# Kernel tuning notes

Hardware: AMD Instinct MI355X
Metric: run time of the kernel (lower is better)

The kernel has to match this reference:

```python
import jax, jax.numpy as jnp
import numpy as np

B, S, D, H, L = 8, 512, 1024, 16, 2
DH = D // H
EPS = 1e-6
SCALE = float(np.sqrt(DH))


def _ln(x, g, b):
    # custom LayerNormalization: unbiased std (torch default), eps added to std
    m = x.mean(axis=-1, keepdims=True)
    s = jnp.std(x, axis=-1, keepdims=True, ddof=1)
    return g * (x - m) / (s + EPS) + b


def _pos_encoding(seq_len, dim):
    pos = jnp.arange(seq_len, dtype=jnp.float32)[:, None]
    dims = jnp.arange(dim, dtype=jnp.float32)
    div = 10000.0 ** (2.0 * dims / dim)
    pe = jnp.zeros((seq_len, dim), jnp.float32)
    pe = pe.at[:, 0::2].set(jnp.sin(pos / div[0::2]))
    pe = pe.at[:, 1::2].set(jnp.cos(pos / div[1::2]))
    return pe


def setup_inputs() -> dict:
    key = jax.random.key(0)
    ks = jax.random.split(key, 20)
    std = 0.02
    p = lambda k, shape: jax.random.normal(k, shape, jnp.float32) * std
    return {
        "features": jax.random.normal(ks[0], (B, S, D), jnp.float32),
        "mask": jnp.ones((B, S), jnp.int32),
        "ln_in_g": jnp.ones((D,), jnp.float32),
        "ln_in_b": jnp.zeros((D,), jnp.float32),
        "Wq": p(ks[1], (L, D, D)), "bq": p(ks[2], (L, D)),
        "Wk": p(ks[3], (L, D, D)), "bk": p(ks[4], (L, D)),
        "Wv": p(ks[5], (L, D, D)), "bv": p(ks[6], (L, D)),
        "Wo": p(ks[7], (L, D, D)), "bo": p(ks[8], (L, D)),
        "ln1_g": jnp.ones((L, D), jnp.float32), "ln1_b": jnp.zeros((L, D), jnp.float32),
        "W1": p(ks[9], (L, D, D)), "b1": p(ks[10], (L, D)),
        "W2": p(ks[11], (L, D, D)), "b2": p(ks[12], (L, D)),
        "ln2_g": jnp.ones((L, D), jnp.float32), "ln2_b": jnp.zeros((L, D), jnp.float32),
    }


def reference(features, mask, ln_in_g, ln_in_b, Wq, bq, Wk, bk, Wv, bv, Wo, bo,
              ln1_g, ln1_b, W1, b1, W2, b2, ln2_g, ln2_b):
    # input norm + positional encoding (dropout inert at eval)
    x = _ln(features, ln_in_g, ln_in_b) + _pos_encoding(S, D)  # [B,S,D]
    # mask: positions where mask==0 are masked out with -1e18
    neg = (mask == 0)[:, None, None, :]  # [B,1,1,Sk]

    def encoder_layer(inp, i):
        q = (inp @ Wq[i].T + bq[i]).reshape(B, S, H, DH).transpose(0, 2, 1, 3)
        k = (inp @ Wk[i].T + bk[i]).reshape(B, S, H, DH).transpose(0, 2, 1, 3)
        v = (inp @ Wv[i].T + bv[i]).reshape(B, S, H, DH).transpose(0, 2, 1, 3)
        scores = jnp.einsum('bhqd,bhkd->bhqk', q, k) / SCALE
        scores = jnp.where(neg, -1e18, scores)
        attn = jax.nn.softmax(scores, axis=-1)
        ctx = jnp.einsum('bhqk,bhkd->bhqd', attn, v).transpose(0, 2, 1, 3).reshape(B, S, D)
        attn_out = ctx @ Wo[i].T + bo[i]
        s = _ln(attn_out + inp, ln1_g[i], ln1_b[i])  # residual + custom LN
        h = jax.nn.gelu(s @ W1[i].T + b1[i], approximate=False)
        f = h @ W2[i].T + b2[i]
        return _ln(f + s, ln2_g[i], ln2_b[i])

    # FAITHFUL to source: layers are NOT chained -- each layer reads the
    # original (query,key,value); output is the last layer's result.
    out = x
    for i in range(L):
        out = encoder_layer(x, i)
    return out
```

## Files before the change

### kernel.cpp

```cpp
#include <hip/hip_runtime.h>
#include <cstdint>
#include <cstddef>


typedef __attribute__((ext_vector_type(8))) short bf16x8;
typedef __attribute__((ext_vector_type(4))) short bf16x4;
typedef __attribute__((ext_vector_type(4))) float f32x4;

#define MFMA16(a, b, c) __builtin_amdgcn_mfma_f32_16x16x32_bf16((a), (b), (c), 0, 0, 0)

__device__ __forceinline__ unsigned short f2b(float f) {
  union { float f; unsigned int u; } x; x.f = f;
  unsigned int r = x.u + 0x7fffu + ((x.u >> 16) & 1u);
  return (unsigned short)(r >> 16);
}

__device__ __forceinline__ float b2f(unsigned short u) {
  union { unsigned int i; float f; } x;
  x.i = ((unsigned int)u) << 16;
  return x.f;
}

__device__ __forceinline__ void gl_lds16(const void* g, void* l) {
  __builtin_amdgcn_global_load_lds(
      (const __attribute__((address_space(1))) void*)g,
      (__attribute__((address_space(3))) void*)l, 16, 0, 0);
}

template <int BN, int EPI>
__global__ __launch_bounds__(256) void gemm_t(
    const unsigned short* __restrict__ A, const unsigned short* __restrict__ B,
    const float* __restrict__ bias, unsigned short* __restrict__ outB, int N,
    int K, int nnHalf) {
  extern __shared__ char smem[];
  char* la = smem;
  char* lb = smem + 3 * 16384;
  constexpr int NR = BN / 32;
  const int tid = threadIdx.x;
  const int l = tid & 63, w = tid >> 6;
  const int l15 = l & 15, l4 = l >> 4;
  const int xcd = blockIdx.x & 7, r = blockIdx.x >> 3;
  const int m0 = ((xcd >> 1) * 8 + (r & 7)) * 128;
  const int n0 = ((xcd & 1) * nnHalf + (r >> 3)) * BN;
  const int wr = (w >> 1) * 64, wc = (w & 1) * (BN / 2);
  const int NT = K >> 6;

#define STAGE(buf, t)                                                         \
  {                                                                           \
    const int k0_ = (t) * 64;                                                 \
    _Pragma("unroll") for (int i = 0; i < 4; ++i) {                           \
      const int c = i * 256 + tid;                                            \
      const int row = c >> 3;                                                 \
      const int gch = (c & 7) ^ (row & 7);                                    \
      gl_lds16(A + (size_t)(m0 + row) * K + k0_ + gch * 8,                    \
               la + (buf) * 16384 + (i * 256 + w * 64) * 16);                 \
    }                                                                         \
    _Pragma("unroll") for (int i = 0; i < BN / 32; ++i) {                     \
      const int c = i * 256 + tid;                                            \
      const int row = c >> 3;                                                 \
      const int gch = (c & 7) ^ (row & 7);                                    \
      gl_lds16(B + (size_t)(n0 + row) * K + k0_ + gch * 8,                    \
               lb + (buf) * (BN * 128) + (i * 256 + w * 64) * 16);            \
    }                                                                         \
  }
#define WAIT_L()                                                   \
  {                                                                \
    if constexpr (BN == 128) {                                     \
      asm volatile("s_waitcnt vmcnt(8)" ::: "memory");             \
    } else {                                                       \
      asm volatile("s_waitcnt vmcnt(6)" ::: "memory");             \
    }                                                              \
  }

  f32x4 acc[4][NR] = {};
  const int sw = l15 & 7;

  STAGE(0, 0);
  STAGE(1, 1);
  WAIT_L();
  __builtin_amdgcn_sched_barrier(0);
  __builtin_amdgcn_s_barrier();
  __builtin_amdgcn_sched_barrier(0);

  for (int t = 0; t < NT; ++t) {
    if (t + 2 < NT) {
      STAGE((t + 2) % 3, t + 2);
    }
    __builtin_amdgcn_sched_barrier(0);
    const char* abuf = la + (t % 3) * 16384;
    const char* bbuf = lb + (t % 3) * (BN * 128);
#pragma unroll
    for (int kk = 0; kk < 2; ++kk) {
      const unsigned int ch = (unsigned int)(((kk * 4 + l4) ^ sw) << 4);
      bf16x8 af[4], bfr[NR];
#pragma unroll
      for (int m = 0; m < 4; ++m)
        af[m] = *(const bf16x8*)(abuf + (wr + m * 16 + l15) * 128 + ch);
#pragma unroll
      for (int n = 0; n < NR; ++n)
        bfr[n] = *(const bf16x8*)(bbuf + (wc + n * 16 + l15) * 128 + ch);
#pragma unroll
      for (int m = 0; m < 4; ++m) {
#pragma unroll
        for (int n = 0; n < NR; ++n) {
          acc[m][n] = MFMA16(af[m], bfr[n], acc[m][n]);
        }
      }
    }
    if (t < NT - 1) {
      if (t + 2 < NT) {
        WAIT_L();
      } else {
        asm volatile("s_waitcnt vmcnt(0)" ::: "memory");
      }
      __builtin_amdgcn_sched_barrier(0);
      __builtin_amdgcn_s_barrier();
      __builtin_amdgcn_sched_barrier(0);
    }
  }
#undef STAGE
#undef WAIT_L

#pragma unroll
  for (int m = 0; m < 4; ++m) {
#pragma unroll
    for (int n = 0; n < NR; ++n) {
      const int col = n0 + wc + n * 16 + l15;
      const float bb = bias[col];
#pragma unroll
      for (int e = 0; e < 4; ++e) {
        const int row = m0 + wr + m * 16 + l4 * 4 + e;
        float v = acc[m][n][e] + bb;
        if (EPI == 1) {
          if (col < 1024) v *= 0.125f;
        } else if (EPI == 2) {
          v = 0.5f * v * (1.f + erff(v * 0.70710678118654752f));
        }
        outB[(size_t)row * N + col] = f2b(v);
      }
    }
  }
}

__global__ __launch_bounds__(256, 2) void attn_kernel(
    const unsigned short* __restrict__ qkv, const int* __restrict__ mask,
    unsigned short* __restrict__ ctx) {
  extern __shared__ char smem[];
  float* maskadd = (float*)(smem + 65536);
  const int bid = blockIdx.x;
  const int b = bid & 7, h = (bid >> 3) & 15, qt = bid >> 7;
  const int tid = threadIdx.x, l = tid & 63, w = tid >> 6;
  const int l15 = l & 15, l4 = l >> 4;
  const size_t RB = (size_t)b * 512 * 3072;

  for (int s = tid; s < 512; s += 256)
    maskadd[s] = mask[b * 512 + s] ? 0.f : -1e18f;

  const unsigned short* Kbase = qkv + RB + 1024 + h * 64;
  const unsigned short* Vbase = qkv + RB + 2048 + h * 64;

  const int kr0 = tid >> 2, kc0 = tid & 3;
  const unsigned int swzk = (unsigned int)((kr0 & 7) << 4);
  const unsigned int ka0 = ((unsigned int)(kr0 * 128 + kc0 * 16)) ^ swzk;
  const unsigned int ka1 = ((unsigned int)(kr0 * 128 + kc0 * 16 + 64)) ^ swzk;
  const int vs0 = 2 * l, vd0 = w * 16;

  bf16x8 k00, k01, k10, k11, vreg[4];
  k00 = *(const bf16x8*)(Kbase + (size_t)kr0 * 3072 + kc0 * 8);
  k01 = *(const bf16x8*)(Kbase + (size_t)kr0 * 3072 + kc0 * 8 + 32);
  k10 = *(const bf16x8*)(Kbase + (size_t)(kr0 + 64) * 3072 + kc0 * 8);
  k11 = *(const bf16x8*)(Kbase + (size_t)(kr0 + 64) * 3072 + kc0 * 8 + 32);
  vreg[0] = *(const bf16x8*)(Vbase + (size_t)vs0 * 3072 + vd0);
  vreg[1] = *(const bf16x8*)(Vbase + (size_t)vs0 * 3072 + vd0 + 8);
  vreg[2] = *(const bf16x8*)(Vbase + (size_t)(vs0 + 1) * 3072 + vd0);
  vreg[3] = *(const bf16x8*)(Vbase + (size_t)(vs0 + 1) * 3072 + vd0 + 8);

  const int q0 = qt * 64 + w * 16;
  const unsigned short* qb =
      qkv + RB + (size_t)(q0 + l15) * 3072 + h * 64 + l4 * 8;
  const bf16x8 qf0 = *(const bf16x8*)(qb);
  const bf16x8 qf1 = *(const bf16x8*)(qb + 32);

#define KWRITE(dst)                        \
  {                                        \
    *(bf16x8*)((dst) + ka0) = k00;         \
    *(bf16x8*)((dst) + ka1) = k01;         \
    *(bf16x8*)((dst) + ka0 + 8192) = k10;  \
    *(bf16x8*)((dst) + ka1 + 8192) = k11;  \
  }
#define VWRITE(dst)                                                          \
  {                                                                          \
    _Pragma("unroll") for (int j = 0; j < 16; ++j) {                         \
      const unsigned short lo_ =                                             \
          (unsigned short)((j < 8) ? vreg[0][j] : vreg[1][j - 8]);           \
      const unsigned short hi_ =                                             \
          (unsigned short)((j < 8) ? vreg[2][j] : vreg[3][j - 8]);           \
      *(unsigned int*)((dst) +                                               \
                       (((vd0 + j) * 256 + vs0 * 2) ^ ((j & 7) << 4))) =     \
          (unsigned int)lo_ | ((unsigned int)hi_ << 16);                     \
    }                                                                        \
  }

  KWRITE(smem);
  VWRITE(smem + 32768);
  __syncthreads();

  const int hi4 = l4 >> 1, gl = l4 & 1, g2 = l4 & 2;
  f32x4 acc[4] = {};
  float run_m = -1e30f, run_s = 0.f;

#pragma unroll
  for (int t = 0; t < 4; ++t) {
    char* kcur = smem + (t & 1) * 16384;
    char* vcur = smem + 32768 + (t & 1) * 16384;
    if (t < 3) {
      const int sn = (t + 1) * 128;
      k00 = *(const bf16x8*)(Kbase + (size_t)(sn + kr0) * 3072 + kc0 * 8);
      k01 = *(const bf16x8*)(Kbase + (size_t)(sn + kr0) * 3072 + kc0 * 8 + 32);
      k10 = *(const bf16x8*)(Kbase + (size_t)(sn + kr0 + 64) * 3072 + kc0 * 8);
      k11 = *(const bf16x8*)(Kbase + (size_t)(sn + kr0 + 64) * 3072 + kc0 * 8 + 32);
      vreg[0] = *(const bf16x8*)(Vbase + (size_t)(sn + vs0) * 3072 + vd0);
      vreg[1] = *(const bf16x8*)(Vbase + (size_t)(sn + vs0) * 3072 + vd0 + 8);
      vreg[2] = *(const bf16x8*)(Vbase + (size_t)(sn + vs0 + 1) * 3072 + vd0);
      vreg[3] = *(const bf16x8*)(Vbase + (size_t)(sn + vs0 + 1) * 3072 + vd0 + 8);
      __builtin_amdgcn_sched_barrier(0);
    }
    f32x4 sc[8];
    __builtin_amdgcn_s_setprio(1);
#pragma unroll
    for (int kk = 0; kk < 8; ++kk) {
      const unsigned int lin = (unsigned int)((kk * 16 + l15) * 128 + l4 * 16);
      const unsigned int swz = (unsigned int)((l15 & 7) << 4);
      const bf16x8 af0 = *(const bf16x8*)(kcur + (lin ^ swz));
      const bf16x8 af1 = *(const bf16x8*)(kcur + ((lin + 64) ^ swz));
      f32x4 c = {0.f, 0.f, 0.f, 0.f};
      c = MFMA16(af0, qf0, c);
      c = MFMA16(af1, qf1, c);
      sc[kk] = c;
    }
    __builtin_amdgcn_s_setprio(0);
    float tmx = -1e30f;
#pragma unroll
    for (int kk = 0; kk < 8; ++kk) {
#pragma unroll
      for (int e = 0; e < 4; ++e) {
        const float v = sc[kk][e] + maskadd[t * 128 + kk * 16 + l4 * 4 + e];
        sc[kk][e] = v;
        tmx = fmaxf(tmx, v);
      }
    }
    tmx = fmaxf(tmx, __shfl_xor(tmx, 16));
    tmx = fmaxf(tmx, __shfl_xor(tmx, 32));
    const float nm = (t == 0) ? tmx : fmaxf(run_m, tmx);
    float tsum = 0.f;
    unsigned int pk[8][2];
#pragma unroll
    for (int kk = 0; kk < 8; ++kk) {
      const float p0 = __expf(sc[kk][0] - nm);
      const float p1 = __expf(sc[kk][1] - nm);
      const float p2 = __expf(sc[kk][2] - nm);
      const float p3 = __expf(sc[kk][3] - nm);
      tsum += (p0 + p1) + (p2 + p3);
      asm("v_cvt_pk_bf16_f32 %0, %1, %2" : "=v"(pk[kk][0]) : "v"(p0), "v"(p1));
      asm("v_cvt_pk_bf16_f32 %0, %1, %2" : "=v"(pk[kk][1]) : "v"(p2), "v"(p3));
    }
    tsum += __shfl_xor(tsum, 16);
    tsum += __shfl_xor(tsum, 32);
    if (t == 0) {
      run_s = tsum;
    } else {
      const float scale = __expf(run_m - nm);
      run_s = run_s * scale + tsum;
      float s4[4];
#pragma unroll
      for (int e = 0; e < 4; ++e) s4[e] = __shfl(scale, l4 * 4 + e);
#pragma unroll
      for (int nt = 0; nt < 4; ++nt) {
#pragma unroll
        for (int e = 0; e < 4; ++e) acc[nt][e] *= s4[e];
      }
    }
    run_m = nm;
#pragma unroll
    for (int k2 = 0; k2 < 4; ++k2) {
      const unsigned int own0 = hi4 ? pk[2 * k2 + 1][0] : pk[2 * k2][0];
      const unsigned int own1 = hi4 ? pk[2 * k2 + 1][1] : pk[2 * k2][1];
      const unsigned int oth0 = hi4 ? pk[2 * k2][0] : pk[2 * k2 + 1][0];
      const unsigned int oth1 = hi4 ? pk[2 * k2][1] : pk[2 * k2 + 1][1];
      const unsigned int s16_0 = (unsigned int)__shfl_xor((int)own0, 16);
      const unsigned int s16_1 = (unsigned int)__shfl_xor((int)own1, 16);
      const unsigned int s32_0 = (unsigned int)__shfl_xor((int)oth0, 32);
      const unsigned int s32_1 = (unsigned int)__shfl_xor((int)oth1, 32);
      const unsigned int s48_0 = (unsigned int)__shfl_xor((int)oth0, 48);
      const unsigned int s48_1 = (unsigned int)__shfl_xor((int)oth1, 48);
      union { unsigned int u[4]; bf16x8 v; } pa;
      pa.u[0] = g2 ? (gl ? s16_0 : s32_0) : (gl ? s48_0 : own0);
      pa.u[1] = g2 ? (gl ? s16_1 : s32_1) : (gl ? s48_1 : own1);
      pa.u[2] = g2 ? (gl ? own0 : s48_0) : (gl ? s32_0 : s16_0);
      pa.u[3] = g2 ? (gl ? own1 : s48_1) : (gl ? s32_1 : s16_1);
      __builtin_amdgcn_s_setprio(1);
#pragma unroll
      for (int nt = 0; nt < 4; ++nt) {
        const int d = nt * 16 + l15;
        const unsigned int vb =
            (unsigned int)((d * 256 + k2 * 64 + l4 * 16) ^ ((l15 & 7) << 4));
        const bf16x8 vbf = *(const bf16x8*)(vcur + vb);
        acc[nt] = MFMA16(pa.v, vbf, acc[nt]);
      }
      __builtin_amdgcn_s_setprio(0);
    }
    if (t < 3) {
      char* knxt = smem + ((t + 1) & 1) * 16384;
      char* vnxt = smem + 32768 + ((t + 1) & 1) * 16384;
      KWRITE(knxt);
      VWRITE(vnxt);
      __syncthreads();
    }
  }
#undef KWRITE
#undef VWRITE

  const float inv = 1.f / run_s;
  float invq[4];
#pragma unroll
  for (int e = 0; e < 4; ++e) invq[e] = __shfl(inv, l4 * 4 + e);
#pragma unroll
  for (int nt = 0; nt < 4; ++nt) {
#pragma unroll
    for (int e = 0; e < 4; ++e) {
      const size_t row = (size_t)b * 512 + q0 + l4 * 4 + e;
      ctx[row * 1024 + h * 64 + nt * 16 + l15] = f2b(acc[nt][e] * invq[e]);
    }
  }
}

template <int MODE>
__global__ __launch_bounds__(256) void ln_k(
    const void* __restrict__ Ap, const void* __restrict__ Rp,
    const float* __restrict__ g, const float* __restrict__ bta,
    void* __restrict__ outp) {
  __shared__ float red[8];
  const int row = blockIdx.x, tid = threadIdx.x;
  const size_t base = (size_t)row * 1024 + tid * 4;
  float a4[4];
  {
    const bf16x4 a = *(const bf16x4*)((const unsigned short*)Ap + base);
    const bf16x4 rr = *(const bf16x4*)((const unsigned short*)Rp + base);
#pragma unroll
    for (int j = 0; j < 4; ++j)
      a4[j] = b2f((unsigned short)a[j]) + b2f((unsigned short)rr[j]);
  }
  float s = a4[0] + a4[1] + a4[2] + a4[3];
  float q = a4[0] * a4[0] + a4[1] * a4[1] + a4[2] * a4[2] + a4[3] * a4[3];
#pragma unroll
  for (int o = 32; o; o >>= 1) {
    s += __shfl_xor(s, o);
    q += __shfl_xor(q, o);
  }
  if ((tid & 63) == 0) {
    red[(tid >> 6) * 2] = s;
    red[(tid >> 6) * 2 + 1] = q;
  }
  __syncthreads();
  const float S = red[0] + red[2] + red[4] + red[6];
  const float Qs = red[1] + red[3] + red[5] + red[7];
  const float mean = S * (1.f / 1024.f);
  float var = (Qs - 1024.f * mean * mean) * (1.f / 1023.f);
  var = fmaxf(var, 0.f);
  const float inv = 1.f / (sqrtf(var) + 1e-6f);
  if (MODE == 2) {
    float4 o4;
    o4.x = g[tid * 4 + 0] * (a4[0] - mean) * inv + bta[tid * 4 + 0];
    o4.y = g[tid * 4 + 1] * (a4[1] - mean) * inv + bta[tid * 4 + 1];
    o4.z = g[tid * 4 + 2] * (a4[2] - mean) * inv + bta[tid * 4 + 2];
    o4.w = g[tid * 4 + 3] * (a4[3] - mean) * inv + bta[tid * 4 + 3];
    *(float4*)((float*)outp + base) = o4;
  } else {
    bf16x4 pb;
#pragma unroll
    for (int j = 0; j < 4; ++j) {
      const int col = tid * 4 + j;
      pb[j] = (short)f2b(g[col] * (a4[j] - mean) * inv + bta[col]);
    }
    *(bf16x4*)((unsigned short*)outp + base) = pb;
  }
}

__global__ __launch_bounds__(256) void prep_ln(
    const float* __restrict__ features, const float* __restrict__ g,
    const float* __restrict__ bta, unsigned short* __restrict__ xb,
    const float* __restrict__ Wq, const float* __restrict__ Wk,
    const float* __restrict__ Wv, const float* __restrict__ Wo,
    const float* __restrict__ W1, const float* __restrict__ W2,
    const float* __restrict__ bq, const float* __restrict__ bk,
    const float* __restrict__ bv, unsigned short* __restrict__ wqkv,
    unsigned short* __restrict__ wo, unsigned short* __restrict__ w1,
    unsigned short* __restrict__ w2, float* __restrict__ bqkv) {
  if (blockIdx.x < 4096) {
    __shared__ float red[8];
    const int row = blockIdx.x, tid = threadIdx.x;
    const size_t base = (size_t)row * 1024 + tid * 4;
    const float4 a = *(const float4*)(features + base);
    float a4[4] = {a.x, a.y, a.z, a.w};
    float s = a4[0] + a4[1] + a4[2] + a4[3];
    float q = a4[0] * a4[0] + a4[1] * a4[1] + a4[2] * a4[2] + a4[3] * a4[3];
#pragma unroll
    for (int o = 32; o; o >>= 1) {
      s += __shfl_xor(s, o);
      q += __shfl_xor(q, o);
    }
    if ((tid & 63) == 0) {
      red[(tid >> 6) * 2] = s;
      red[(tid >> 6) * 2 + 1] = q;
    }
    __syncthreads();
    const float S = red[0] + red[2] + red[4] + red[6];
    const float Qs = red[1] + red[3] + red[5] + red[7];
    const float mean = S * (1.f / 1024.f);
    float var = (Qs - 1024.f * mean * mean) * (1.f / 1023.f);
    var = fmaxf(var, 0.f);
    const float inv = 1.f / (sqrtf(var) + 1e-6f);
    bf16x4 pb;
#pragma unroll
    for (int j = 0; j < 4; ++j) {
      const int col = tid * 4 + j;
      float y = g[col] * (a4[j] - mean) * inv + bta[col];
      const float ang =
          (float)(row & 511) * exp2f((float)col * -0.025952563241307518f);
      y += (col & 1) ? cosf(ang) : sinf(ang);
      pb[j] = (short)f2b(y);
    }
    *(bf16x4*)(xb + base) = pb;
  } else {
    const int gid = (blockIdx.x - 4096) * 256 + threadIdx.x;
    if (gid < 1572864) {
      const int chunk = gid >> 18;
      const int off = (gid & 262143) * 4;
      const float* s;
      unsigned short* d;
      switch (chunk) {
        case 0: s = Wq; d = wqkv; break;
        case 1: s = Wk; d = wqkv + 1048576; break;
        case 2: s = Wv; d = wqkv + 2097152; break;
        case 3: s = Wo; d = wo; break;
        case 4: s = W1; d = w1; break;
        default: s = W2; d = w2; break;
      }
      const float4 v = *(const float4*)(s + off);
      bf16x4 o;
      o[0] = (short)f2b(v.x); o[1] = (short)f2b(v.y);
      o[2] = (short)f2b(v.z); o[3] = (short)f2b(v.w);
      *(bf16x4*)(d + off) = o;
    } else {
      const int idx = (gid - 1572864) * 4;
      if (idx < 3072) {
        const float* bs = idx < 1024 ? bq : (idx < 2048 ? bk - 1024 : bv - 2048);
        *(float4*)(bqkv + idx) = *(const float4*)(bs + idx);
      }
    }
  }
}

extern "C" void kernel_launch(void* const* d_in, const int* in_sizes, int n_in,
                              void* d_out, int out_size, void* d_ws, size_t ws_size,
                              hipStream_t stream) {
  (void)in_sizes; (void)n_in; (void)out_size; (void)ws_size;
  const float* features = (const float*)d_in[0];
  const int* mask = (const int*)d_in[1];
  const float* ln_in_g = (const float*)d_in[2];
  const float* ln_in_b = (const float*)d_in[3];
  const size_t DD = 1024 * 1024;
  const float* Wq = (const float*)d_in[4] + DD;
  const float* bq = (const float*)d_in[5] + 1024;
  const float* Wk = (const float*)d_in[6] + DD;
  const float* bk = (const float*)d_in[7] + 1024;
  const float* Wv = (const float*)d_in[8] + DD;
  const float* bv = (const float*)d_in[9] + 1024;
  const float* Wo = (const float*)d_in[10] + DD;
  const float* bo = (const float*)d_in[11] + 1024;
  const float* l1g = (const float*)d_in[12] + 1024;
  const float* l1b = (const float*)d_in[13] + 1024;
  const float* W1 = (const float*)d_in[14] + DD;
  const float* b1 = (const float*)d_in[15] + 1024;
  const float* W2 = (const float*)d_in[16] + DD;
  const float* b2 = (const float*)d_in[17] + 1024;
  const float* l2g = (const float*)d_in[18] + 1024;
  const float* l2b = (const float*)d_in[19] + 1024;

  char* base = (char*)d_ws;
  unsigned short* qkv = (unsigned short*)(base);
  unsigned short* xb = (unsigned short*)(base + 25165824);
  unsigned short* ctxb = (unsigned short*)(base + 33554432);
  unsigned short* abuf = (unsigned short*)(base + 41943040);
  unsigned short* wqkv = (unsigned short*)(base + 50331648);
  unsigned short* wo = (unsigned short*)(base + 56623104);
  unsigned short* w1 = (unsigned short*)(base + 58720256);
  unsigned short* w2 = (unsigned short*)(base + 60817408);
  float* bqkv = (float*)(base + 62914560);

  hipFuncSetAttribute((const void*)gemm_t<128, 1>,
                      hipFuncAttributeMaxDynamicSharedMemorySize, 98304);
  hipFuncSetAttribute((const void*)gemm_t<64, 2>,
                      hipFuncAttributeMaxDynamicSharedMemorySize, 73728);
  hipFuncSetAttribute((const void*)gemm_t<64, 3>,
                      hipFuncAttributeMaxDynamicSharedMemorySize, 73728);
  hipFuncSetAttribute((const void*)attn_kernel,
                      hipFuncAttributeMaxDynamicSharedMemorySize, 67584);

  prep_ln<<<4096 + 6147, 256, 0, stream>>>(
      features, ln_in_g, ln_in_b, xb, Wq, Wk, Wv, Wo, W1, W2, bq, bk, bv,
      wqkv, wo, w1, w2, bqkv);
  gemm_t<128, 1><<<768, 256, 98304, stream>>>(xb, wqkv, bqkv, qkv, 3072, 1024, 12);
  attn_kernel<<<1024, 256, 67584, stream>>>(qkv, mask, ctxb);
  gemm_t<64, 3><<<512, 256, 73728, stream>>>(ctxb, wo, bo, abuf, 1024, 1024, 8);
  ln_k<1><<<4096, 256, 0, stream>>>(abuf, xb, l1g, l1b, ctxb);
  gemm_t<64, 2><<<512, 256, 73728, stream>>>(ctxb, w1, b1, xb, 1024, 1024, 8);
  gemm_t<64, 3><<<512, 256, 73728, stream>>>(xb, w2, b2, abuf, 1024, 1024, 8);
  ln_k<2><<<4096, 256, 0, stream>>>(abuf, ctxb, l2g, l2b, (float*)d_out);
}
```

Before: 152.9 us.

## Store QKV head-major from GEMM epilogue and stage K via direct global-to-LDS loads

The QKV projection epilogue now writes Q, K and V into a [tensor][head][batch][seq][64] contiguous layout instead of a row-major [B*S,3072] matrix. The attention kernel reads from this layout, so each head's rows are contiguous. K tiles are now loaded with direct global_load_lds into swizzled LDS instead of going through registers, which drops the register round trip and separate LDS writes. The cost is scattered 2-byte stores in the GEMM epilogue, and the K prefetch into the other buffer is now an async write that depends on the existing barrier placement.

New measurement: 152.6 us. Within noise of the previous version (-0.2%).

```diff
diff --git a/kernel.cpp b/kernel.cpp
--- a/kernel.cpp
+++ b/kernel.cpp
@@ -132,11 +132,20 @@
         const int row = m0 + wr + m * 16 + l4 * 4 + e;
         float v = acc[m][n][e] + bb;
         if (EPI == 1) {
-          if (col < 1024) v *= 0.125f;
-        } else if (EPI == 2) {
-          v = 0.5f * v * (1.f + erff(v * 0.70710678118654752f));
+          const int tsr = col >> 10;
+          const int hh = (col >> 6) & 15;
+          const int dh = col & 63;
+          if (tsr == 0) v *= 0.125f;
+          const size_t off =
+              (((size_t)((tsr * 16 + hh) * 8 + (row >> 9))) << 15) +
+              ((size_t)(row & 511) << 6) + dh;
+          outB[off] = f2b(v);
+        } else {
+          if (EPI == 2) {
+            v = 0.5f * v * (1.f + erff(v * 0.70710678118654752f));
+          }
+          outB[(size_t)row * N + col] = f2b(v);
         }
-        outB[(size_t)row * N + col] = f2b(v);
       }
     }
   }
@@ -151,42 +160,33 @@
   const int b = bid & 7, h = (bid >> 3) & 15, qt = bid >> 7;
   const int tid = threadIdx.x, l = tid & 63, w = tid >> 6;
   const int l15 = l & 15, l4 = l >> 4;
-  const size_t RB = (size_t)b * 512 * 3072;
 
   for (int s = tid; s < 512; s += 256)
     maskadd[s] = mask[b * 512 + s] ? 0.f : -1e18f;
 
-  const unsigned short* Kbase = qkv + RB + 1024 + h * 64;
-  const unsigned short* Vbase = qkv + RB + 2048 + h * 64;
-
-  const int kr0 = tid >> 2, kc0 = tid & 3;
-  const unsigned int swzk = (unsigned int)((kr0 & 7) << 4);
-  const unsigned int ka0 = ((unsigned int)(kr0 * 128 + kc0 * 16)) ^ swzk;
-  const unsigned int ka1 = ((unsigned int)(kr0 * 128 + kc0 * 16 + 64)) ^ swzk;
+  const unsigned short* Qb = qkv + (((size_t)(h * 8 + b)) << 15);
+  const unsigned short* Kb = qkv + (((size_t)((16 + h) * 8 + b)) << 15);
+  const unsigned short* Vb = qkv + (((size_t)((32 + h) * 8 + b)) << 15);
+
+#define STAGE_K(dstbuf, sn_)                                          \
+  {                                                                   \
+    _Pragma("unroll") for (int i = 0; i < 4; ++i) {                   \
+      const int c = i * 256 + tid;                                    \
+      const int row = c >> 3;                                         \
+      const int gch = (c & 7) ^ (row & 7);                            \
+      gl_lds16(Kb + (size_t)((sn_) + row) * 64 + gch * 8,             \
+               (dstbuf) + c * 16);                                    \
+    }                                                                 \
+  }
+
   const int vs0 = 2 * l, vd0 = w * 16;
-
-  bf16x8 k00, k01, k10, k11, vreg[4];
-  k00 = *(const bf16x8*)(Kbase + (size_t)kr0 * 3072 + kc0 * 8);
-  k01 = *(const bf16x8*)(Kbase + (size_t)kr0 * 3072 + kc0 * 8 + 32);
-  k10 = *(const bf16x8*)(Kbase + (size_t)(kr0 + 64) * 3072 + kc0 * 8);
-  k11 = *(const bf16x8*)(Kbase + (size_t)(kr0 + 64) * 3072 + kc0 * 8 + 32);
-  vreg[0] = *(const bf16x8*)(Vbase + (size_t)vs0 * 3072 + vd0);
-  vreg[1] = *(const bf16x8*)(Vbase + (size_t)vs0 * 3072 + vd0 + 8);
-  vreg[2] = *(const bf16x8*)(Vbase + (size_t)(vs0 + 1) * 3072 + vd0);
-  vreg[3] = *(const bf16x8*)(Vbase + (size_t)(vs0 + 1) * 3072 + vd0 + 8);
-
-  const int q0 = qt * 64 + w * 16;
-  const unsigned short* qb =
-      qkv + RB + (size_t)(q0 + l15) * 3072 + h * 64 + l4 * 8;
-  const bf16x8 qf0 = *(const bf16x8*)(qb);
-  const bf16x8 qf1 = *(const bf16x8*)(qb + 32);
-
-#define KWRITE(dst)                        \
-  {                                        \
-    *(bf16x8*)((dst) + ka0) = k00;         \
-    *(bf16x8*)((dst) + ka1) = k01;         \
-    *(bf16x8*)((dst) + ka0 + 8192) = k10;  \
-    *(bf16x8*)((dst) + ka1 + 8192) = k11;  \
+  bf16x8 vreg[4];
+#define VLOAD(sn_)                                                          \
+  {                                                                         \
+    vreg[0] = *(const bf16x8*)(Vb + (size_t)((sn_) + vs0) * 64 + vd0);      \
+    vreg[1] = *(const bf16x8*)(Vb + (size_t)((sn_) + vs0) * 64 + vd0 + 8);  \
+    vreg[2] = *(const bf16x8*)(Vb + (size_t)((sn_) + vs0 + 1) * 64 + vd0);  \
+    vreg[3] = *(const bf16x8*)(Vb + (size_t)((sn_) + vs0 + 1) * 64 + vd0 + 8); \
   }
 #define VWRITE(dst)                                                          \
   {                                                                          \
@@ -201,7 +201,13 @@
     }                                                                        \
   }
 
-  KWRITE(smem);
+  const int q0 = qt * 64 + w * 16;
+  const unsigned short* qb = Qb + (size_t)(q0 + l15) * 64 + l4 * 8;
+  const bf16x8 qf0 = *(const bf16x8*)(qb);
+  const bf16x8 qf1 = *(const bf16x8*)(qb + 32);
+
+  STAGE_K(smem, 0);
+  VLOAD(0);
   VWRITE(smem + 32768);
   __syncthreads();
 
@@ -213,16 +219,12 @@
   for (int t = 0; t < 4; ++t) {
     char* kcur = smem + (t & 1) * 16384;
     char* vcur = smem + 32768 + (t & 1) * 16384;
+    char* knxt = smem + ((t + 1) & 1) * 16384;
+    char* vnxt = smem + 32768 + ((t + 1) & 1) * 16384;
     if (t < 3) {
       const int sn = (t + 1) * 128;
-      k00 = *(const bf16x8*)(Kbase + (size_t)(sn + kr0) * 3072 + kc0 * 8);
-      k01 = *(const bf16x8*)(Kbase + (size_t)(sn + kr0) * 3072 + kc0 * 8 + 32);
-      k10 = *(const bf16x8*)(Kbase + (size_t)(sn + kr0 + 64) * 3072 + kc0 * 8);
-      k11 = *(const bf16x8*)(Kbase + (size_t)(sn + kr0 + 64) * 3072 + kc0 * 8 + 32);
-      vreg[0] = *(const bf16x8*)(Vbase + (size_t)(sn + vs0) * 3072 + vd0);
-      vreg[1] = *(const bf16x8*)(Vbase + (size_t)(sn + vs0) * 3072 + vd0 + 8);
-      vreg[2] = *(const bf16x8*)(Vbase + (size_t)(sn + vs0 + 1) * 3072 + vd0);
-      vreg[3] = *(const bf16x8*)(Vbase + (size_t)(sn + vs0 + 1) * 3072 + vd0 + 8);
+      STAGE_K(knxt, sn);
+      VLOAD(sn);
       __builtin_amdgcn_sched_barrier(0);
     }
     f32x4 sc[8];
@@ -310,14 +312,12 @@
       __builtin_amdgcn_s_setprio(0);
     }
     if (t < 3) {
-      char* knxt = smem + ((t + 1) & 1) * 16384;
-      char* vnxt = smem + 32768 + ((t + 1) & 1) * 16384;
-      KWRITE(knxt);
       VWRITE(vnxt);
       __syncthreads();
     }
   }
-#undef KWRITE
+#undef STAGE_K
+#undef VLOAD
 #undef VWRITE
 
   const float inv = 1.f / run_s;
```
